# Performance work log

Measured on AMD Instinct MI355X. Metric: run time of the kernel, lower is better.

The kernel has to match this reference:

```python
import jax, jax.numpy as jnp
import numpy as np
import math

B, T, H, NH, BLOCK = 2, 2048, 1024, 16, 2048
HS = H // NH  # 64, even as required by RoPE


def make_rope_cache(hs, block):
    # positions t = 1..block (note: source starts at 1, not 0)
    t = np.arange(1, block + 1, dtype=np.float32)[:, None]          # (block, 1)
    i = np.arange(1, hs // 2 + 1, dtype=np.float32)[None, :]        # (1, hs/2)
    theta = (1.0 / 10000.0) ** (2.0 * (i - 1.0) / hs)               # (1, hs/2)
    ang = t * theta                                                  # (block, hs/2)
    return jnp.asarray(np.stack([np.cos(ang), np.sin(ang)], axis=-1))  # (block, hs/2, 2)


def setup_inputs() -> dict:
    key = jax.random.key(0)
    ks = jax.random.split(key, 10)
    s = 0.02
    x = jax.random.normal(ks[0], (B, T, H), jnp.float32)
    masks = jax.random.randint(ks[1], (B, T), 0, 2, jnp.int32)  # 1 = padding token
    Wq = jax.random.normal(ks[2], (H, H), jnp.float32) * s
    bq = jnp.zeros((H,), jnp.float32)
    Wk = jax.random.normal(ks[3], (H, H), jnp.float32) * s
    bk = jnp.zeros((H,), jnp.float32)
    Wv = jax.random.normal(ks[4], (H, H), jnp.float32) * s
    bv = jnp.zeros((H,), jnp.float32)
    Wo = jax.random.normal(ks[5], (H, H), jnp.float32) * s  # final_proj, no bias
    rope = make_rope_cache(HS, BLOCK)
    return {"x": x, "masks": masks, "Wq": Wq, "bq": bq, "Wk": Wk, "bk": bk,
            "Wv": Wv, "bv": bv, "Wo": Wo, "rope": rope}


def _apply_rope(x, cos, sin):
    # x: (B, nh, T, hs); cos/sin: (T, hs/2) broadcast over (B, nh)
    xe, xo = x[..., ::2], x[..., 1::2]
    real = cos * xe - sin * xo
    imag = sin * xe + cos * xo
    return jnp.stack([real, imag], axis=-1).reshape(x.shape)


def reference(x, masks, Wq, bq, Wk, bk, Wv, bv, Wo, rope):
    Bn, Tn, Hn = x.shape
    nh, hs = NH, Hn // NH

    def proj(W, b):
        # torch Linear: x @ W.T + b -> (B, nh, T, hs)
        return (x @ W.T + b).reshape(Bn, Tn, nh, hs).transpose(0, 2, 1, 3)

    Q, K, V = proj(Wq, bq), proj(Wk, bk), proj(Wv, bv)
    cos, sin = rope[:Tn, :, 0], rope[:Tn, :, 1]
    Q = _apply_rope(Q, cos, sin)
    K = _apply_rope(K, cos, sin)

    att = jnp.einsum('bhqd,bhkd->bhqk', Q, K) * (1.0 / math.sqrt(hs))
    causal = jnp.tril(jnp.ones((Tn, Tn), bool))
    att = jnp.where(causal[None, None, :, :], att, -1e10)          # causal mask
    att = jnp.where((masks == 1)[:, None, None, :], -1e10, att)   # padding mask on keys
    att = jax.nn.softmax(att, axis=-1)

    y = jnp.einsum('bhqk,bhkd->bhqd', att, V)
    y = y.transpose(0, 2, 1, 3).reshape(Bn, Tn, Hn)
    return y @ Wo.T  # final_proj has no bias
```

## Files before the change

kernel.cpp:

```cpp
#include <hip/hip_runtime.h>

typedef short short8 __attribute__((ext_vector_type(8)));
typedef float floatx4 __attribute__((ext_vector_type(4)));
typedef unsigned short u16;
typedef unsigned long long u64;

#define Tn 2048
#define Kdim 1024
#define QSCALE 0.18033688011112042f
#define FIXEDMAX 20.0f

__device__ inline u16 f2bf(float x) {
    union { float f; unsigned u; } c; c.f = x;
    unsigned u = c.u;
    u += 0x7fffu + ((u >> 16) & 1u);
    return (u16)(u >> 16);
}
__device__ inline float bf2f(u16 h) {
    union { unsigned u; float f; } c; c.u = ((unsigned)h) << 16;
    return c.f;
}
__device__ inline floatx4 mfma16(short8 a, short8 b, floatx4 c) {
    return __builtin_amdgcn_mfma_f32_16x16x32_bf16(a, b, c, 0, 0, 0);
}
__device__ inline void async16(const void* g, void* l) {
    __builtin_amdgcn_global_load_lds((const __attribute__((address_space(1))) void*)g,
                                     (__attribute__((address_space(3))) void*)l, 16, 0, 0);
}

__global__ __launch_bounds__(256) void cvt_all_k(
    const float* __restrict__ x, const float* __restrict__ wq, const float* __restrict__ wk,
    const float* __restrict__ wv, const float* __restrict__ wo, u16* __restrict__ dst)
{
    int i = blockIdx.x * 256 + threadIdx.x;
    const float* s; int off;
    if (i < 1048576) { s = x; off = i; }
    else {
        int j = i - 1048576; int seg = j >> 18; off = j & 262143;
        s = (seg == 0) ? wq : (seg == 1) ? wk : (seg == 2) ? wv : wo;
    }
    float4 v = ((const float4*)s)[off];
    u64 pk = (u64)f2bf(v.x) | ((u64)f2bf(v.y) << 16) | ((u64)f2bf(v.z) << 32) | ((u64)f2bf(v.w) << 48);
    ((u64*)dst)[i] = pk;
}

__global__ __launch_bounds__(256, 5) void gemm_qkv_k(
    const u16* __restrict__ A,
    const u16* __restrict__ W0, const u16* __restrict__ W1, const u16* __restrict__ W2,
    const float* __restrict__ b0, const float* __restrict__ b1, const float* __restrict__ b2,
    u16* o0, u16* o1, u16* o2,
    const float2* __restrict__ rope)
{
    int z = blockIdx.z;
    const u16* W = (z == 0) ? W0 : (z == 1 ? W1 : W2);
    const float* bias = (z == 0) ? b0 : (z == 1 ? b1 : b2);
    u16* outp = (z == 0) ? o0 : (z == 1 ? o1 : o2);

    __shared__ __align__(16) char lds[24576];
    int tid = threadIdx.x;
    int w = tid >> 6, lane = tid & 63, quad = lane >> 4, l15 = lane & 15;
    int m0 = blockIdx.y * 128, n0 = blockIdx.x * 64;
    int wm = w * 32;

    floatx4 acc[2][4];
    floatx4 vzero = {0.f, 0.f, 0.f, 0.f};
#pragma unroll
    for (int i = 0; i < 2; ++i)
#pragma unroll
        for (int j = 0; j < 4; ++j) acc[i][j] = vzero;

    for (int k0 = 0; k0 < Kdim; k0 += 64) {
#pragma unroll
        for (int j = 0; j < 4; ++j) {
            int f = j * 256 + tid, r = f >> 3, c = (f & 7) ^ (r & 7);
            async16(A + (size_t)(m0 + r) * Kdim + k0 + c * 8, lds + j * 4096 + w * 1024);
        }
#pragma unroll
        for (int j = 0; j < 2; ++j) {
            int f = j * 256 + tid, r = f >> 3, c = (f & 7) ^ (r & 7);
            async16(W + (size_t)(n0 + r) * Kdim + k0 + c * 8, lds + 16384 + j * 4096 + w * 1024);
        }
        __syncthreads();
        short8 af[2][2];
#pragma unroll
        for (int mt = 0; mt < 2; ++mt) {
            int ra = wm + mt * 16 + l15;
            const char* pa = lds + ra * 128;
#pragma unroll
            for (int ks = 0; ks < 2; ++ks)
                af[mt][ks] = *(const short8*)(pa + (((ks * 4 + quad) ^ (ra & 7)) << 4));
        }
#pragma unroll
        for (int ks = 0; ks < 2; ++ks)
#pragma unroll
            for (int nt = 0; nt < 4; ++nt) {
                int rb = nt * 16 + l15;
                short8 bf = *(const short8*)(lds + 16384 + rb * 128 + (((ks * 4 + quad) ^ (rb & 7)) << 4));
                acc[0][nt] = mfma16(af[0][ks], bf, acc[0][nt]);
                acc[1][nt] = mfma16(af[1][ks], bf, acc[1][nt]);
            }
        __syncthreads();
    }

    int mbase = m0 + wm;
    if (z <= 1) {
        float osc = (z == 0) ? QSCALE : 1.0f;
#pragma unroll
        for (int nt = 0; nt < 4; ++nt) {
            int col = n0 + nt * 16 + l15;
            float bv = bias[col];
            int p = (col & 63) >> 1;
#pragma unroll
            for (int mt = 0; mt < 2; ++mt) {
                floatx4 a = acc[mt][nt];
#pragma unroll
                for (int r = 0; r < 4; ++r) {
                    int row = mbase + mt * 16 + quad * 4 + r;
                    float v = a[r] + bv;
                    float ov = __shfl_xor(v, 1, 64);
                    float2 cs = rope[(row & (Tn - 1)) * 32 + p];
                    float res = (cs.x * v + ((lane & 1) ? cs.y * ov : -cs.y * ov)) * osc;
                    float pres = __shfl_xor(res, 1, 64);
                    if (!(lane & 1)) {
                        unsigned pk = (unsigned)f2bf(res) | ((unsigned)f2bf(pres) << 16);
                        *(unsigned*)(outp + (size_t)row * 1024 + col) = pk;
                    }
                }
            }
        }
    } else {
#pragma unroll
        for (int nt = 0; nt < 4; ++nt) {
            int col = n0 + nt * 16 + l15;
            float bv = bias[col];
#pragma unroll
            for (int mt = 0; mt < 2; ++mt) {
                floatx4 a = acc[mt][nt];
                int row0 = mbase + mt * 16 + quad * 4;
                int bb = row0 >> 11, t0 = row0 & (Tn - 1);
                u64 pk = (u64)f2bf(a[0] + bv) | ((u64)f2bf(a[1] + bv) << 16)
                       | ((u64)f2bf(a[2] + bv) << 32) | ((u64)f2bf(a[3] + bv) << 48);
                *(u64*)(outp + (size_t)(bb * 1024 + col) * Tn + t0) = pk;
            }
        }
    }
}

__global__ __launch_bounds__(256, 4) void gemm_o_k(
    const u16* __restrict__ A, const u16* __restrict__ W, float* __restrict__ out)
{
    __shared__ __align__(16) char lds[16384];
    int tid = threadIdx.x;
    int w = tid >> 6, lane = tid & 63, quad = lane >> 4, l15 = lane & 15;
    int m0 = blockIdx.y * 64, n0 = blockIdx.x * 64;
    int wm = (w >> 1) * 32, wn = (w & 1) * 32;

    floatx4 acc[2][2];
    floatx4 vzero = {0.f, 0.f, 0.f, 0.f};
#pragma unroll
    for (int i = 0; i < 2; ++i)
#pragma unroll
        for (int j = 0; j < 2; ++j) acc[i][j] = vzero;

    for (int k0 = 0; k0 < Kdim; k0 += 64) {
#pragma unroll
        for (int j = 0; j < 2; ++j) {
            int f = j * 256 + tid, r = f >> 3, c = (f & 7) ^ (r & 7);
            async16(A + (size_t)(m0 + r) * Kdim + k0 + c * 8, lds + j * 4096 + w * 1024);
            async16(W + (size_t)(n0 + r) * Kdim + k0 + c * 8, lds + 8192 + j * 4096 + w * 1024);
        }
        __syncthreads();
        short8 af[2][2];
#pragma unroll
        for (int mt = 0; mt < 2; ++mt) {
            int ra = wm + mt * 16 + l15;
            const char* pa = lds + ra * 128;
#pragma unroll
            for (int ks = 0; ks < 2; ++ks)
                af[mt][ks] = *(const short8*)(pa + (((ks * 4 + quad) ^ (ra & 7)) << 4));
        }
#pragma unroll
        for (int ks = 0; ks < 2; ++ks)
#pragma unroll
            for (int nt = 0; nt < 2; ++nt) {
                int rb = wn + nt * 16 + l15;
                short8 bf = *(const short8*)(lds + 8192 + rb * 128 + (((ks * 4 + quad) ^ (rb & 7)) << 4));
                acc[0][nt] = mfma16(af[0][ks], bf, acc[0][nt]);
                acc[1][nt] = mfma16(af[1][ks], bf, acc[1][nt]);
            }
        __syncthreads();
    }

#pragma unroll
    for (int nt = 0; nt < 2; ++nt) {
        int col = n0 + wn + nt * 16 + l15;
#pragma unroll
        for (int mt = 0; mt < 2; ++mt) {
            floatx4 a = acc[mt][nt];
#pragma unroll
            for (int r = 0; r < 4; ++r) {
                int row = m0 + wm + mt * 16 + quad * 4 + r;
                out[(size_t)row * 1024 + col] = a[r];
            }
        }
    }
}

__global__ __launch_bounds__(64) void vmean_k(const u16* __restrict__ Vt, float* __restrict__ vmean) {
    int row = blockIdx.x;
    int lane = threadIdx.x;
    const u16* p = Vt + (size_t)row * Tn;
    float s = 0.f;
    for (int i = lane * 8; i < Tn; i += 512) {
        short8 v = *(const short8*)(p + i);
#pragma unroll
        for (int j = 0; j < 8; ++j) s += bf2f((u16)v[j]);
    }
#pragma unroll
    for (int off = 1; off < 64; off <<= 1) s += __shfl_xor(s, off, 64);
    if (lane == 0) vmean[row] = s * (1.f / 2048.f);
}

__global__ __launch_bounds__(256) void flash_k(
    const u16* __restrict__ Qb, const u16* __restrict__ Kb, const u16* __restrict__ Vt,
    const int* __restrict__ masks, const float* __restrict__ vmean, u16* __restrict__ Yb)
{
    int bid = blockIdx.x;
    int bh = (bid & 7) * 4 + ((bid >> 3) & 3);
    int qt = 31 - (bid >> 5);
    int b = bh >> 4, h = bh & 15;
    int tid = threadIdx.x, w = tid >> 6, lane = tid & 63, quad = lane >> 4, l15 = lane & 15;
    int sc = (lane & 7) ^ (lane >> 3);

    __shared__ __align__(16) u16 ldsK[2][64 * 64];
    __shared__ __align__(16) u16 ldsV[2][64 * 64];
    __shared__ __align__(16) u16 ldsP[4][16 * 64];

    int ktiles = qt + 1;
    unsigned blo = 0, bhi = 0;
    for (int j = 0; j < ktiles; ++j) {
        u64 mk = __ballot(masks[b * Tn + j * 64 + lane] != 0);
        if (lane == j) { blo = (unsigned)mk; bhi = (unsigned)(mk >> 32); }
    }

    auto stage = [&](int bb, int k0) {
#pragma unroll
        for (int j = 0; j < 2; ++j) {
            int row = j * 32 + w * 8 + (lane >> 3);
            const u16* gk = Kb + (size_t)(b * Tn + k0 + row) * 1024 + h * 64 + sc * 8;
            async16(gk, (char*)&ldsK[bb][0] + (j * 32 + w * 8) * 128);
            const u16* gv = Vt + (size_t)(b * 1024 + h * 64 + row) * Tn + k0 + sc * 8;
            async16(gv, (char*)&ldsV[bb][0] + (j * 32 + w * 8) * 128);
        }
    };
    floatx4 vzero = {0.f, 0.f, 0.f, 0.f};

    int q0 = qt * 64 + w * 16;
    short8 qf[2];
    {
        const u16* qp = Qb + (size_t)(b * Tn + q0 + l15) * 1024 + h * 64 + quad * 8;
        qf[0] = *(const short8*)qp;
        qf[1] = *(const short8*)(qp + 32);
    }
    floatx4 o[4];
    float lsum[4] = {0.f, 0.f, 0.f, 0.f};
#pragma unroll
    for (int i = 0; i < 4; ++i) o[i] = vzero;

    stage(0, 0);
    for (int kt = 0; kt < ktiles; ++kt) {
        int k0 = kt * 64;
        int bb = kt & 1;
        __syncthreads();

        short8 kf[4][2], vf[4][2];
#pragma unroll
        for (int f = 0; f < 4; ++f) {
            int key = f * 16 + l15;
            const char* kbase = (const char*)&ldsK[bb][0] + key * 128;
            const char* vbase = (const char*)&ldsV[bb][0] + key * 128;
#pragma unroll
            for (int ks = 0; ks < 2; ++ks) {
                int slot = ((quad + ks * 4) ^ (key & 7)) << 4;
                kf[f][ks] = *(const short8*)(kbase + slot);
                vf[f][ks] = *(const short8*)(vbase + slot);
            }
        }
        if (kt + 1 < ktiles) stage(bb ^ 1, k0 + 64);

        floatx4 s[4];
#pragma unroll
        for (int f = 0; f < 4; ++f) {
            s[f] = mfma16(qf[0], kf[f][0], vzero);
            s[f] = mfma16(qf[1], kf[f][1], s[f]);
        }

        unsigned mlo = __shfl(blo, kt, 64), mhi = __shfl(bhi, kt, 64);
        int mb[4];
        mb[0] = (mlo >> l15) & 1; mb[1] = (mlo >> (l15 + 16)) & 1;
        mb[2] = (mhi >> l15) & 1; mb[3] = (mhi >> (l15 + 16)) & 1;

        if (k0 + 63 <= q0) {
#pragma unroll
            for (int r = 0; r < 4; ++r) {
                float psum = 0.f;
#pragma unroll
                for (int f = 0; f < 4; ++f) {
                    float v = mb[f] ? -1e10f : s[f][r];
                    float p = __builtin_amdgcn_exp2f(v - FIXEDMAX);
                    psum += p;
                    unsigned u = __float_as_uint(p) + 0x8000u;
                    int row = quad * 4 + r, key = f * 16 + l15;
                    ldsP[w][0] = ldsP[w][0];
                    *((u16*)((char*)&ldsP[w][0] + row * 128 +
                             ((((key >> 3) ^ (row & 7))) << 4) + (key & 7) * 2)) = (u16)(u >> 16);
                }
                lsum[r] += psum;
            }
        } else {
#pragma unroll
            for (int r = 0; r < 4; ++r) {
                int lim = q0 + quad * 4 + r - k0;
                float psum = 0.f;
#pragma unroll
                for (int f = 0; f < 4; ++f) {
                    float v = (16 * f + l15 > lim || mb[f]) ? -1e10f : s[f][r];
                    float p = __builtin_amdgcn_exp2f(v - FIXEDMAX);
                    psum += p;
                    unsigned u = __float_as_uint(p) + 0x8000u;
                    int row = quad * 4 + r, key = f * 16 + l15;
                    *((u16*)((char*)&ldsP[w][0] + row * 128 +
                             ((((key >> 3) ^ (row & 7))) << 4) + (key & 7) * 2)) = (u16)(u >> 16);
                }
                lsum[r] += psum;
            }
        }
        __asm__ volatile("s_waitcnt lgkmcnt(0)" ::: "memory");
        short8 pf0 = *(const short8*)((const char*)&ldsP[w][0] + l15 * 128 + ((quad ^ (l15 & 7)) << 4));
        short8 pf1 = *(const short8*)((const char*)&ldsP[w][0] + l15 * 128 + (((quad + 4) ^ (l15 & 7)) << 4));
#pragma unroll
        for (int nb = 0; nb < 4; ++nb) {
            o[nb] = mfma16(pf0, vf[nb][0], o[nb]);
            o[nb] = mfma16(pf1, vf[nb][1], o[nb]);
        }
    }

#pragma unroll
    for (int r = 0; r < 4; ++r) {
        int qq = q0 + quad * 4 + r;
        float l = lsum[r];
#pragma unroll
        for (int off = 1; off < 16; off <<= 1) l += __shfl_xor(l, off, 64);
        bool degen = (l == 0.f);
        float linv = 1.0f / l;
#pragma unroll
        for (int nb = 0; nb < 4; ++nb) {
            int d = nb * 16 + l15;
            float val = degen ? vmean[b * 1024 + h * 64 + d] : o[nb][r] * linv;
            float pv = __shfl_xor(val, 1, 64);
            if (!(lane & 1)) {
                unsigned pk = (unsigned)f2bf(val) | ((unsigned)f2bf(pv) << 16);
                *(unsigned*)(Yb + (size_t)(b * Tn + qq) * 1024 + h * 64 + d) = pk;
            }
        }
    }
}

extern "C" void kernel_launch(void* const* d_in, const int* in_sizes, int n_in,
                              void* d_out, int out_size, void* d_ws, size_t ws_size,
                              hipStream_t stream) {
    const float* x  = (const float*)d_in[0];
    const int* masks = (const int*)d_in[1];
    const float* Wq = (const float*)d_in[2];
    const float* bq = (const float*)d_in[3];
    const float* Wk = (const float*)d_in[4];
    const float* bk = (const float*)d_in[5];
    const float* Wv = (const float*)d_in[6];
    const float* bv = (const float*)d_in[7];
    const float* Wo = (const float*)d_in[8];
    const float2* rope = (const float2*)d_in[9];
    float* out = (float*)d_out;

    char* ws = (char*)d_ws;
    u16* xb   = (u16*)(ws);
    u16* Wqb  = (u16*)(ws + (8  << 20));
    u16* Wkb  = (u16*)(ws + (10 << 20));
    u16* Wvb  = (u16*)(ws + (12 << 20));
    u16* Wob  = (u16*)(ws + (14 << 20));
    u16* Qb   = (u16*)(ws + (16 << 20));
    u16* Kb2  = (u16*)(ws + (24 << 20));
    u16* Vt   = (u16*)(ws + (32 << 20));
    u16* Yb   = (u16*)(ws + (40 << 20));
    float* vm = (float*)(ws + (48 << 20));

    cvt_all_k<<<8192, 256, 0, stream>>>(x, Wq, Wk, Wv, Wo, xb);

    gemm_qkv_k<<<dim3(16, 32, 3), 256, 0, stream>>>(xb, Wqb, Wkb, Wvb, bq, bk, bv,
                                                    Qb, Kb2, Vt, rope);
    vmean_k<<<2048, 64, 0, stream>>>(Vt, vm);
    flash_k<<<1024, 256, 0, stream>>>(Qb, Kb2, Vt, masks, vm, Yb);
    gemm_o_k<<<dim3(16, 64), 256, 0, stream>>>(Yb, Wob, out);
}
```

Baseline: 195.5 us.

## Pair causal query tiles per block to balance work and reuse K/V tiles

Each flash-attention block now processes two query tiles, qt and 31-qt, sharing the same staged K/V tiles from LDS. This balances causal work so every block does 33 tile iterations and halves K/V global loads per query, with the grid halved to 512 blocks. The cost is more registers (two accumulator sets), extra LDS for a second P buffer, and fewer blocks, which may lower occupancy and latency hiding.

```diff
diff --git a/kernel.cpp b/kernel.cpp
--- a/kernel.cpp
+++ b/kernel.cpp
@@ -227,16 +227,18 @@
 {
     int bid = blockIdx.x;
     int bh = (bid & 7) * 4 + ((bid >> 3) & 3);
-    int qt = 31 - (bid >> 5);
+    int pr = bid >> 5;
+    int qtA = 31 - pr, qtB = pr;
     int b = bh >> 4, h = bh & 15;
     int tid = threadIdx.x, w = tid >> 6, lane = tid & 63, quad = lane >> 4, l15 = lane & 15;
     int sc = (lane & 7) ^ (lane >> 3);
 
     __shared__ __align__(16) u16 ldsK[2][64 * 64];
     __shared__ __align__(16) u16 ldsV[2][64 * 64];
-    __shared__ __align__(16) u16 ldsP[4][16 * 64];
-
-    int ktiles = qt + 1;
+    __shared__ __align__(16) u16 ldsPA[4][16 * 64];
+    __shared__ __align__(16) u16 ldsPB[4][16 * 64];
+
+    int ktiles = qtA + 1;
     unsigned blo = 0, bhi = 0;
     for (int j = 0; j < ktiles; ++j) {
         u64 mk = __ballot(masks[b * Tn + j * 64 + lane] != 0);
@@ -255,17 +257,22 @@
     };
     floatx4 vzero = {0.f, 0.f, 0.f, 0.f};
 
-    int q0 = qt * 64 + w * 16;
-    short8 qf[2];
+    int q0A = qtA * 64 + w * 16;
+    int q0B = qtB * 64 + w * 16;
+    short8 qfA[2], qfB[2];
     {
-        const u16* qp = Qb + (size_t)(b * Tn + q0 + l15) * 1024 + h * 64 + quad * 8;
-        qf[0] = *(const short8*)qp;
-        qf[1] = *(const short8*)(qp + 32);
-    }
-    floatx4 o[4];
-    float lsum[4] = {0.f, 0.f, 0.f, 0.f};
-#pragma unroll
-    for (int i = 0; i < 4; ++i) o[i] = vzero;
+        const u16* qp = Qb + (size_t)(b * Tn + q0A + l15) * 1024 + h * 64 + quad * 8;
+        qfA[0] = *(const short8*)qp;
+        qfA[1] = *(const short8*)(qp + 32);
+        const u16* qq = Qb + (size_t)(b * Tn + q0B + l15) * 1024 + h * 64 + quad * 8;
+        qfB[0] = *(const short8*)qq;
+        qfB[1] = *(const short8*)(qq + 32);
+    }
+    floatx4 oA[4], oB[4];
+    float lsumA[4] = {0.f, 0.f, 0.f, 0.f};
+    float lsumB[4] = {0.f, 0.f, 0.f, 0.f};
+#pragma unroll
+    for (int i = 0; i < 4; ++i) { oA[i] = vzero; oB[i] = vzero; }
 
     stage(0, 0);
     for (int kt = 0; kt < ktiles; ++kt) {
@@ -288,67 +295,120 @@
         }
         if (kt + 1 < ktiles) stage(bb ^ 1, k0 + 64);
 
-        floatx4 s[4];
-#pragma unroll
-        for (int f = 0; f < 4; ++f) {
-            s[f] = mfma16(qf[0], kf[f][0], vzero);
-            s[f] = mfma16(qf[1], kf[f][1], s[f]);
-        }
-
         unsigned mlo = __shfl(blo, kt, 64), mhi = __shfl(bhi, kt, 64);
         int mb[4];
         mb[0] = (mlo >> l15) & 1; mb[1] = (mlo >> (l15 + 16)) & 1;
         mb[2] = (mhi >> l15) & 1; mb[3] = (mhi >> (l15 + 16)) & 1;
 
-        if (k0 + 63 <= q0) {
-#pragma unroll
-            for (int r = 0; r < 4; ++r) {
-                float psum = 0.f;
-#pragma unroll
-                for (int f = 0; f < 4; ++f) {
-                    float v = mb[f] ? -1e10f : s[f][r];
-                    float p = __builtin_amdgcn_exp2f(v - FIXEDMAX);
-                    psum += p;
-                    unsigned u = __float_as_uint(p) + 0x8000u;
-                    int row = quad * 4 + r, key = f * 16 + l15;
-                    ldsP[w][0] = ldsP[w][0];
-                    *((u16*)((char*)&ldsP[w][0] + row * 128 +
-                             ((((key >> 3) ^ (row & 7))) << 4) + (key & 7) * 2)) = (u16)(u >> 16);
+        {
+            floatx4 s[4];
+#pragma unroll
+            for (int f = 0; f < 4; ++f) {
+                s[f] = mfma16(qfA[0], kf[f][0], vzero);
+                s[f] = mfma16(qfA[1], kf[f][1], s[f]);
+            }
+            if (k0 + 63 <= q0A) {
+#pragma unroll
+                for (int r = 0; r < 4; ++r) {
+                    float psum = 0.f;
+#pragma unroll
+                    for (int f = 0; f < 4; ++f) {
+                        float v = mb[f] ? -1e10f : s[f][r];
+                        float p = __builtin_amdgcn_exp2f(v - FIXEDMAX);
+                        psum += p;
+                        unsigned u = __float_as_uint(p) + 0x8000u;
+                        int row = quad * 4 + r, key = f * 16 + l15;
+                        *((u16*)((char*)&ldsPA[w][0] + row * 128 +
+                                 ((((key >> 3) ^ (row & 7))) << 4) + (key & 7) * 2)) = (u16)(u >> 16);
+                    }
+                    lsumA[r] += psum;
                 }
-                lsum[r] += psum;
-            }
-        } else {
-#pragma unroll
-            for (int r = 0; r < 4; ++r) {
-                int lim = q0 + quad * 4 + r - k0;
-                float psum = 0.f;
-#pragma unroll
-                for (int f = 0; f < 4; ++f) {
-                    float v = (16 * f + l15 > lim || mb[f]) ? -1e10f : s[f][r];
-                    float p = __builtin_amdgcn_exp2f(v - FIXEDMAX);
-                    psum += p;
-                    unsigned u = __float_as_uint(p) + 0x8000u;
-                    int row = quad * 4 + r, key = f * 16 + l15;
-                    *((u16*)((char*)&ldsP[w][0] + row * 128 +
-                             ((((key >> 3) ^ (row & 7))) << 4) + (key & 7) * 2)) = (u16)(u >> 16);
+            } else {
+#pragma unroll
+                for (int r = 0; r < 4; ++r) {
+                    int lim = q0A + quad * 4 + r - k0;
+                    float psum = 0.f;
+#pragma unroll
+                    for (int f = 0; f < 4; ++f) {
+                        float v = (16 * f + l15 > lim || mb[f]) ? -1e10f : s[f][r];
+                        float p = __builtin_amdgcn_exp2f(v - FIXEDMAX);
+                        psum += p;
+                        unsigned u = __float_as_uint(p) + 0x8000u;
+                        int row = quad * 4 + r, key = f * 16 + l15;
+                        *((u16*)((char*)&ldsPA[w][0] + row * 128 +
+                                 ((((key >> 3) ^ (row & 7))) << 4) + (key & 7) * 2)) = (u16)(u >> 16);
+                    }
+                    lsumA[r] += psum;
                 }
-                lsum[r] += psum;
+            }
+        }
+        if (kt <= qtB) {
+            floatx4 s[4];
+#pragma unroll
+            for (int f = 0; f < 4; ++f) {
+                s[f] = mfma16(qfB[0], kf[f][0], vzero);
+                s[f] = mfma16(qfB[1], kf[f][1], s[f]);
+            }
+            if (k0 + 63 <= q0B) {
+#pragma unroll
+                for (int r = 0; r < 4; ++r) {
+                    float psum = 0.f;
+#pragma unroll
+                    for (int f = 0; f < 4; ++f) {
+                        float v = mb[f] ? -1e10f : s[f][r];
+                        float p = __builtin_amdgcn_exp2f(v - FIXEDMAX);
+                        psum += p;
+                        unsigned u = __float_as_uint(p) + 0x8000u;
+                        int row = quad * 4 + r, key = f * 16 + l15;
+                        *((u16*)((char*)&ldsPB[w][0] + row * 128 +
+                                 ((((key >> 3) ^ (row & 7))) << 4) + (key & 7) * 2)) = (u16)(u >> 16);
+                    }
+                    lsumB[r] += psum;
+                }
+            } else {
+#pragma unroll
+                for (int r = 0; r < 4; ++r) {
+                    int lim = q0B + quad * 4 + r - k0;
+                    float psum = 0.f;
+#pragma unroll
+                    for (int f = 0; f < 4; ++f) {
+                        float v = (16 * f + l15 > lim || mb[f]) ? -1e10f : s[f][r];
+                        float p = __builtin_amdgcn_exp2f(v - FIXEDMAX);
+                        psum += p;
+                        unsigned u = __float_as_uint(p) + 0x8000u;
+                        int row = quad * 4 + r, key = f * 16 + l15;
+                        *((u16*)((char*)&ldsPB[w][0] + row * 128 +
+                                 ((((key >> 3) ^ (row & 7))) << 4) + (key & 7) * 2)) = (u16)(u >> 16);
+                    }
+                    lsumB[r] += psum;
+                }
             }
         }
         __asm__ volatile("s_waitcnt lgkmcnt(0)" ::: "memory");
-        short8 pf0 = *(const short8*)((const char*)&ldsP[w][0] + l15 * 128 + ((quad ^ (l15 & 7)) << 4));
-        short8 pf1 = *(const short8*)((const char*)&ldsP[w][0] + l15 * 128 + (((quad + 4) ^ (l15 & 7)) << 4));
-#pragma unroll
-        for (int nb = 0; nb < 4; ++nb) {
-            o[nb] = mfma16(pf0, vf[nb][0], o[nb]);
-            o[nb] = mfma16(pf1, vf[nb][1], o[nb]);
+        {
+            short8 pf0 = *(const short8*)((const char*)&ldsPA[w][0] + l15 * 128 + ((quad ^ (l15 & 7)) << 4));
+            short8 pf1 = *(const short8*)((const char*)&ldsPA[w][0] + l15 * 128 + (((quad + 4) ^ (l15 & 7)) << 4));
+#pragma unroll
+            for (int nb = 0; nb < 4; ++nb) {
+                oA[nb] = mfma16(pf0, vf[nb][0], oA[nb]);
+                oA[nb] = mfma16(pf1, vf[nb][1], oA[nb]);
+            }
+        }
+        if (kt <= qtB) {
+            short8 pf0 = *(const short8*)((const char*)&ldsPB[w][0] + l15 * 128 + ((quad ^ (l15 & 7)) << 4));
+            short8 pf1 = *(const short8*)((const char*)&ldsPB[w][0] + l15 * 128 + (((quad + 4) ^ (l15 & 7)) << 4));
+#pragma unroll
+            for (int nb = 0; nb < 4; ++nb) {
+                oB[nb] = mfma16(pf0, vf[nb][0], oB[nb]);
+                oB[nb] = mfma16(pf1, vf[nb][1], oB[nb]);
+            }
         }
     }
 
 #pragma unroll
     for (int r = 0; r < 4; ++r) {
-        int qq = q0 + quad * 4 + r;
-        float l = lsum[r];
+        int qq = q0A + quad * 4 + r;
+        float l = lsumA[r];
 #pragma unroll
         for (int off = 1; off < 16; off <<= 1) l += __shfl_xor(l, off, 64);
         bool degen = (l == 0.f);
@@ -356,7 +416,26 @@
 #pragma unroll
         for (int nb = 0; nb < 4; ++nb) {
             int d = nb * 16 + l15;
-            float val = degen ? vmean[b * 1024 + h * 64 + d] : o[nb][r] * linv;
+            float val = degen ? vmean[b * 1024 + h * 64 + d] : oA[nb][r] * linv;
+            float pv = __shfl_xor(val, 1, 64);
+            if (!(lane & 1)) {
+                unsigned pk = (unsigned)f2bf(val) | ((unsigned)f2bf(pv) << 16);
+                *(unsigned*)(Yb + (size_t)(b * Tn + qq) * 1024 + h * 64 + d) = pk;
+            }
+        }
+    }
+#pragma unroll
+    for (int r = 0; r < 4; ++r) {
+        int qq = q0B + quad * 4 + r;
+        float l = lsumB[r];
+#pragma unroll
+        for (int off = 1; off < 16; off <<= 1) l += __shfl_xor(l, off, 64);
+        bool degen = (l == 0.f);
+        float linv = 1.0f / l;
+#pragma unroll
+        for (int nb = 0; nb < 4; ++nb) {
+            int d = nb * 16 + l15;
+            float val = degen ? vmean[b * 1024 + h * 64 + d] : oB[nb][r] * linv;
             float pv = __shfl_xor(val, 1, 64);
             if (!(lane & 1)) {
                 unsigned pk = (unsigned)f2bf(val) | ((unsigned)f2bf(pv) << 16);
@@ -398,6 +477,6 @@
     gemm_qkv_k<<<dim3(16, 32, 3), 256, 0, stream>>>(xb, Wqb, Wkb, Wvb, bq, bk, bv,
                                                     Qb, Kb2, Vt, rope);
     vmean_k<<<2048, 64, 0, stream>>>(Vt, vm);
-    flash_k<<<1024, 256, 0, stream>>>(Qb, Kb2, Vt, masks, vm, Yb);
+    flash_k<<<512, 256, 0, stream>>>(Qb, Kb2, Vt, masks, vm, Yb);
     gemm_o_k<<<dim3(16, 64), 256, 0, stream>>>(Yb, Wob, out);
 }
```

Result: slower. 204.3 us (+4.5%).
